# Kernel optimization log

Hardware: AMD Instinct MI355X
Metric: run time of the kernel (lower is better)

The kernel has to match this reference:

```python
import jax, jax.numpy as jnp
import numpy as np


def _shift(w):
    # max(0, -min(w)): scalar shift making w + shift non-negative
    return jnp.maximum(0.0, -jnp.min(w))


def shifted_linear(x, W, b=None):
    # F.linear with non-negative weights plus row-sum correction
    alpha = _shift(W)
    y = x @ (W + alpha).T - alpha * jnp.sum(x, axis=-1, keepdims=True)
    if b is not None:
        y = y + b
    return y


def shifted_depthwise_conv(x, w, b):
    # x: (B, D, L), w: (D, 1, K) depthwise; causal-style padding K-1, sliced to L by caller
    alpha = _shift(w)
    k = w.shape[2]
    pad = k - 1
    dn = ('NCH', 'OIH', 'NCH')
    groups = w.shape[0]
    y = jax.lax.conv_general_dilated(x, w + alpha, (1,), [(pad, pad)],
                                     dimension_numbers=dn, feature_group_count=groups)
    ones_k = jnp.ones_like(w)
    ssum = jax.lax.conv_general_dilated(x, ones_k, (1,), [(pad, pad)],
                                        dimension_numbers=dn, feature_group_count=groups)
    return y - alpha * ssum + b[None, :, None]


def setup_inputs() -> dict:
    key = jax.random.key(0)
    ks = jax.random.split(key, 10)
    d_model, d_inner, d_state, d_conv, dt_rank = 1024, 2048, 16, 4, 64
    B, L = 2, 1024
    s = 0.05
    return {
        'hidden_states': jax.random.normal(ks[0], (B, L, d_model), jnp.float32),
        'W_in': jax.random.normal(ks[1], (2 * d_inner, d_model), jnp.float32) * s,
        'conv_w': jax.random.normal(ks[2], (d_inner, 1, d_conv), jnp.float32) * 0.3,
        'conv_b': jax.random.normal(ks[3], (d_inner,), jnp.float32) * s,
        'W_x': jax.random.normal(ks[4], (dt_rank + 2 * d_state, d_inner), jnp.float32) * s,
        'W_dt': jax.random.normal(ks[5], (d_inner, dt_rank), jnp.float32) * s,
        'dt_bias': jax.random.normal(ks[6], (d_inner,), jnp.float32),
        'W_out': jax.random.normal(ks[7], (d_model, d_inner), jnp.float32) * s,
        'A_log': jax.random.normal(ks[8], (d_inner, d_state), jnp.float32) * 0.5,
        'D': jax.random.normal(ks[9], (d_inner,), jnp.float32),
    }


def reference(hidden_states, W_in, conv_w, conv_b, W_x, W_dt, dt_bias, W_out, A_log, D):
    b, l, dm = hidden_states.shape
    d_inner = conv_w.shape[0]
    d_state = A_log.shape[1]
    dt_rank = W_dt.shape[1]

    A = jnp.exp(A_log)  # (d_inner, d_state), always positive

    # in_proj over (b*l, d_model) -> (b, 2*d_inner, l)
    xz = shifted_linear(hidden_states.reshape(b * l, dm), W_in)
    xz = xz.reshape(b, l, 2 * d_inner).transpose(0, 2, 1)
    x, z = xz[:, :d_inner], xz[:, d_inner:]

    # depthwise shifted conv + SiLU activation, truncated to seqlen
    x = jax.nn.silu(shifted_depthwise_conv(x, conv_w, conv_b)[..., :l])

    # x_proj -> dt_raw, B, C
    x_dbl = shifted_linear(x.transpose(0, 2, 1).reshape(b * l, d_inner), W_x)
    dt_raw = x_dbl[:, :dt_rank]
    Bm = x_dbl[:, dt_rank:dt_rank + d_state].reshape(b, l, d_state).transpose(0, 2, 1)  # (b,n,l)
    Cm = x_dbl[:, dt_rank + d_state:].reshape(b, l, d_state).transpose(0, 2, 1)         # (b,n,l)
    dt = shifted_linear(dt_raw, W_dt).reshape(b, l, d_inner).transpose(0, 2, 1)          # (b,d,l)

    # delta activation (softplus) with bias, clamped
    delta = jnp.clip(jax.nn.softplus(dt + dt_bias[None, :, None]), 1e-4, 20.0)

    # global scalar shifts for B and C
    beta = _shift(Bm)
    gamma = _shift(Cm)
    B_nn = Bm + beta
    C_nn = Cm + gamma

    # precomputed per-step operands, scan axis first: (l, b, d, n)
    deltaA = jnp.exp(-jnp.einsum('bdl,dn->lbdn', delta, A))
    dBu = jnp.einsum('bdl,bnl,bdl->lbdn', delta, B_nn, x)
    C_scan = C_nn.transpose(2, 0, 1)  # (l, b, n)

    def step(xc, inp):
        dA_i, dBu_i, C_i = inp
        xc = dA_i * xc + dBu_i                                   # (b,d,n)
        y = jnp.einsum('bdn,bn->bd', xc, C_i) - gamma * jnp.sum(xc, axis=-1)
        return xc, y

    x0 = jnp.zeros((b, d_inner, d_state), dtype=delta.dtype)
    _, ys = jax.lax.scan(step, x0, (deltaA, dBu, C_scan))        # ys: (l, b, d)

    y = ys.transpose(1, 2, 0) + x * D[None, :, None]             # (b, d, l) skip term
    y = y * jax.nn.silu(z)                                       # gate activation

    out = shifted_linear(y.transpose(0, 2, 1).reshape(b * l, d_inner), W_out)
    return out.reshape(b, l, dm)
```

## Files before the change

### kernel.cpp

```cpp
#include <hip/hip_runtime.h>
#include <hip/hip_bf16.h>
#include <math.h>

#define DM 1024
#define DI 2048
#define DS 16
#define DTR 64
#define NB 2
#define LL 1024
#define TT (NB*LL)
#define SCH 32
#define NCH (LL/SCH)

typedef unsigned short u16;
typedef __attribute__((ext_vector_type(8))) short bf16x8;
typedef __attribute__((ext_vector_type(4))) float f32x4;

#define LOG2E 1.4426950408889634f

__device__ inline u16 f2bf(float f) {
  union { float f; unsigned u; } c; c.f = f;
  unsigned u = c.u;
  return (u16)((u + 0x7fffu + ((u >> 16) & 1u)) >> 16);
}
__device__ inline float bf2f(u16 u) {
  union { unsigned u; float f; } c; c.u = ((unsigned)u) << 16;
  return c.f;
}

__device__ inline unsigned fkey(float f) {
  union { float f; unsigned u; } c; c.f = f;
  return (c.u & 0x80000000u) ? ~c.u : (c.u | 0x80000000u);
}
__device__ inline float funkey(unsigned k) {
  union { unsigned u; float f; } c;
  c.u = (k & 0x80000000u) ? (k & 0x7fffffffu) : ~k;
  return c.f;
}

#define GLDS16(g, l) __builtin_amdgcn_global_load_lds( \
    (const __attribute__((address_space(1))) unsigned int*)(g), \
    (__attribute__((address_space(3))) unsigned int*)(l), 16, 0, 0)

template<int BM, int BN, int EPI, int OB, int CG = 0>
__global__ __launch_bounds__(256) void gemm_bf16(
    const u16* __restrict__ A, const u16* __restrict__ B,
    void* __restrict__ Cv, int M, int N, int K, int kpb,
    const float* __restrict__ bias) {
  constexpr int WAVES_M = BM / 64;
  constexpr int WAVES_N = 4 / WAVES_M;
  constexpr int WTM = 4;
  constexpr int WTN = BN / (WAVES_N * 16);
  constexpr int ASLABS = BM / 16;
  constexpr int SLABS = (BM + BN) / 16;
  constexpr int SPW = SLABS / 4;
  __shared__ u16 As[BM * 32];
  __shared__ u16 Bs[BN * 32];
  const int tid = threadIdx.x;
  const int wave = tid >> 6;
  const int lane = tid & 63;
  const int bm = blockIdx.y * BM;
  const int bn = blockIdx.x * BN;
  const int wm = (wave / WAVES_N) * 64;
  const int wn = (wave % WAVES_N) * (WTN * 16);
  const int r4 = lane >> 2;
  const int kc = (lane & 3) * 8;
  const int fr = lane & 15;
  const int fq = lane >> 4;
  const int koff = blockIdx.z * kpb;
  float* C = (float*)Cv + (OB == 0 ? (size_t)blockIdx.z * M * N : (size_t)0);
  u16* C16 = (u16*)Cv;

  f32x4 acc[WTM][WTN];
#pragma unroll
  for (int i = 0; i < WTM; ++i)
#pragma unroll
    for (int j = 0; j < WTN; ++j) acc[i][j] = (f32x4){0.f, 0.f, 0.f, 0.f};

  for (int k0 = koff; k0 < koff + kpb; k0 += 32) {
#pragma unroll
    for (int s = wave * SPW; s < (wave + 1) * SPW; ++s) {
      if (s < ASLABS) {
        int row = s * 16 + r4;
        GLDS16(A + (size_t)(bm + row) * K + k0 + kc, &As[s * 512]);
      } else {
        int row = (s - ASLABS) * 16 + r4;
        GLDS16(B + (size_t)(bn + row) * K + k0 + kc, &Bs[(s - ASLABS) * 512]);
      }
    }
    __syncthreads();
    bf16x8 af[WTM], bf[WTN];
#pragma unroll
    for (int i = 0; i < WTM; ++i)
      af[i] = *(const bf16x8*)&As[(wm + 16 * i + fr) * 32 + fq * 8];
#pragma unroll
    for (int j = 0; j < WTN; ++j)
      bf[j] = *(const bf16x8*)&Bs[(wn + 16 * j + fr) * 32 + fq * 8];
#pragma unroll
    for (int i = 0; i < WTM; ++i)
#pragma unroll
      for (int j = 0; j < WTN; ++j)
        acc[i][j] = __builtin_amdgcn_mfma_f32_16x16x32_bf16(af[i], bf[j], acc[i][j], 0, 0, 0);
    __syncthreads();
  }

#pragma unroll
  for (int i = 0; i < WTM; ++i) {
    int row0 = bm + wm + 16 * i + fq * 4;
#pragma unroll
    for (int j = 0; j < WTN; ++j) {
      int col = bn + wn + 16 * j + fr;
#pragma unroll
      for (int r = 0; r < 4; ++r) {
        float v = acc[i][j][r];
        if (EPI == 1) {
          v += bias[col];
          float sp = (v > 20.0f) ? v : log1pf(expf(v));
          v = fminf(fmaxf(sp, 1e-4f), 20.0f);
        }
        if (OB == 1) {
          C16[(size_t)(row0 + r) * N + col] = f2bf(v);
        } else if (OB == 2) {
          if (CG == 0 || col < CG) {
            const int ldc = (CG > 0) ? CG : N;
            atomicAdd(&C[(size_t)(row0 + r) * ldc + col], v);
          }
        } else {
          C[(size_t)(row0 + r) * N + col] = v;
        }
      }
    }
  }
}

__global__ __launch_bounds__(256) void dtbeta(
    const float* __restrict__ xdb, u16* __restrict__ dtraw_bf,
    unsigned* __restrict__ betakey) {
  const int t0 = blockIdx.x * 32;
  const int tid = threadIdx.x;
#pragma unroll
  for (int i = tid; i < 32 * 64; i += 256) {
    int t = t0 + (i >> 6), c = i & 63;
    dtraw_bf[t * 64 + c] = f2bf(xdb[t * 96 + c]);
  }
  float mn = 3.4e38f;
#pragma unroll
  for (int i = tid; i < 32 * 16; i += 256) {
    int t = t0 + (i >> 4), n = i & 15;
    mn = fminf(mn, xdb[t * 96 + 64 + n]);
  }
#pragma unroll
  for (int o = 32; o; o >>= 1) mn = fminf(mn, __shfl_down(mn, o));
  __shared__ float sm[4];
  if ((tid & 63) == 0) sm[tid >> 6] = mn;
  __syncthreads();
  if (tid == 0) {
    float m = fminf(fminf(sm[0], sm[1]), fminf(sm[2], sm[3]));
    atomicMin(betakey, fkey(m));
  }
}

__global__ __launch_bounds__(256) void cast_all(
    const float* __restrict__ hs, const float* __restrict__ win,
    const float* __restrict__ wout, const float* __restrict__ wx,
    const float* __restrict__ wdt,
    u16* __restrict__ hs_bf, u16* __restrict__ win_bf,
    u16* __restrict__ wout_bf, u16* __restrict__ wx_bf,
    u16* __restrict__ wdt_bf, float* __restrict__ xdb,
    float* __restrict__ outz, unsigned* __restrict__ betakey) {
  int gid = blockIdx.x * 256 + threadIdx.x;
  if (gid == 0) betakey[0] = 0xFFFFFFFFu;
  const float* src; u16* dst; int off;
  if (gid < 524288)       { src = hs;   dst = hs_bf;   off = gid; }
  else if (gid < 1572864) { src = win;  dst = win_bf;  off = gid - 524288; }
  else if (gid < 2097152) { src = wout; dst = wout_bf; off = gid - 1572864; }
  else if (gid < 2146304) { src = wx;   dst = wx_bf;   off = gid - 2097152; }
  else if (gid < 2179072) { src = wdt;  dst = wdt_bf;  off = gid - 2146304; }
  else if (gid < 2195456) {
    ushort4 z4 = {0, 0, 0, 0};
    ((ushort4*)wx_bf)[49152 + gid - 2179072] = z4;
    return;
  } else if (gid < 2244608) {
    float4 z = {0.f, 0.f, 0.f, 0.f};
    ((float4*)xdb)[gid - 2195456] = z;
    return;
  } else {
    float4 z = {0.f, 0.f, 0.f, 0.f};
    ((float4*)outz)[gid - 2244608] = z;
    return;
  }
  float4 v = ((const float4*)src)[off];
  ushort4 o;
  o.x = f2bf(v.x); o.y = f2bf(v.y); o.z = f2bf(v.z); o.w = f2bf(v.w);
  ((ushort4*)dst)[off] = o;
}

__global__ __launch_bounds__(256) void conv_silu4(
    const u16* __restrict__ xz, const float* __restrict__ w,
    const float* __restrict__ cb, u16* __restrict__ xc_bf) {
  int gid = blockIdx.x * 256 + threadIdx.x;
  int dq = (gid & 511) * 4;
  int t = gid >> 9;
  int l = t & (LL - 1);
  float wv[4][4];
#pragma unroll
  for (int j = 0; j < 4; ++j) {
    float4 ww = *(const float4*)&w[(dq + j) * 4];
    wv[j][0] = ww.x; wv[j][1] = ww.y; wv[j][2] = ww.z; wv[j][3] = ww.w;
  }
  float4 acc = *(const float4*)&cb[dq];
#pragma unroll
  for (int k = 0; k < 4; ++k) {
    int ll = l - 3 + k;
    if (ll < 0) continue;
    ushort4 xv = *(const ushort4*)&xz[(size_t)(t - 3 + k) * (2 * DI) + dq];
    acc.x += bf2f(xv.x) * wv[0][k]; acc.y += bf2f(xv.y) * wv[1][k];
    acc.z += bf2f(xv.z) * wv[2][k]; acc.w += bf2f(xv.w) * wv[3][k];
  }
  acc.x /= (1.0f + expf(-acc.x)); acc.y /= (1.0f + expf(-acc.y));
  acc.z /= (1.0f + expf(-acc.z)); acc.w /= (1.0f + expf(-acc.w));
  ushort4 o;
  o.x = f2bf(acc.x); o.y = f2bf(acc.y); o.z = f2bf(acc.z); o.w = f2bf(acc.w);
  *(ushort4*)&xc_bf[(size_t)t * DI + dq] = o;
}

__global__ __launch_bounds__(256) void scan_pass1(
    const u16* __restrict__ delta, const u16* __restrict__ xc_bf,
    const float* __restrict__ xdb, const float* __restrict__ A_log,
    const unsigned* __restrict__ betak,
    float* __restrict__ hend, float* __restrict__ Ssum) {
  const int d = blockIdx.x * 256 + threadIdx.x;
  const int c = blockIdx.y;
  const int b = blockIdx.z;
  __shared__ float Bsh[SCH][16];
  const float beta = fmaxf(0.0f, -funkey(betak[0]));
  const int t0 = b * LL + c * SCH;
  for (int i = threadIdx.x; i < SCH * 16; i += 256) {
    int tt = i >> 4, n = i & 15;
    Bsh[tt][n] = xdb[(size_t)(t0 + tt) * 96 + 64 + n] + beta;
  }
  __syncthreads();
  float Av2[16];
#pragma unroll
  for (int n = 0; n < 16; ++n) Av2[n] = expf(A_log[d * 16 + n]) * LOG2E;
  float h[16];
#pragma unroll
  for (int n = 0; n < 16; ++n) h[n] = 0.f;
  float S = 0.f;
  for (int tt = 0; tt < SCH; ++tt) {
    int t = t0 + tt;
    float dv = bf2f(delta[(size_t)t * DI + d]);
    float xv = bf2f(xc_bf[(size_t)t * DI + d]);
    float dx = dv * xv;
    S += dv;
#pragma unroll
    for (int n = 0; n < 16; ++n) {
      float a = __builtin_amdgcn_exp2f(-dv * Av2[n]);
      h[n] = a * h[n] + dx * Bsh[tt][n];
    }
  }
  size_t base = (((size_t)(b * NCH + c) * DI) + d) * 16;
#pragma unroll
  for (int n = 0; n < 16; ++n) hend[base + n] = h[n];
  Ssum[((size_t)(b * NCH + c) * DI) + d] = S;
}

__global__ __launch_bounds__(256) void scan_pass2(
    float* __restrict__ hend, const float* __restrict__ Ssum,
    const float* __restrict__ A_log) {
  int gid = blockIdx.x * 256 + threadIdx.x;
  int n = gid & 15;
  int d = (gid >> 4) & (DI - 1);
  int b = gid >> 15;
  float Av2 = expf(A_log[d * 16 + n]) * LOG2E;
  float H = 0.f;
  for (int c = 0; c < NCH; ++c) {
    size_t cb = ((size_t)(b * NCH + c) * DI) + d;
    float hl = hend[cb * 16 + n];
    float p = __builtin_amdgcn_exp2f(-Av2 * Ssum[cb]);
    hend[cb * 16 + n] = H;
    H = p * H + hl;
  }
}

__global__ __launch_bounds__(256) void scan_pass3(
    const u16* __restrict__ delta, const u16* __restrict__ xc_bf,
    const float* __restrict__ xdb, const u16* __restrict__ xz_bf,
    const float* __restrict__ A_log, const float* __restrict__ Dp,
    const unsigned* __restrict__ betak, const float* __restrict__ hstart,
    u16* __restrict__ ybf) {
  const int d = blockIdx.x * 256 + threadIdx.x;
  const int c = blockIdx.y;
  const int b = blockIdx.z;
  __shared__ float Bsh[SCH][16];
  __shared__ float Csh[SCH][16];
  const float beta = fmaxf(0.0f, -funkey(betak[0]));
  const int t0 = b * LL + c * SCH;
  for (int i = threadIdx.x; i < SCH * 16; i += 256) {
    int tt = i >> 4, n = i & 15;
    size_t row = (size_t)(t0 + tt) * 96;
    Bsh[tt][n] = xdb[row + 64 + n] + beta;
    Csh[tt][n] = xdb[row + 80 + n];
  }
  __syncthreads();
  float Av2[16];
#pragma unroll
  for (int n = 0; n < 16; ++n) Av2[n] = expf(A_log[d * 16 + n]) * LOG2E;
  float h[16];
  size_t base = (((size_t)(b * NCH + c) * DI) + d) * 16;
#pragma unroll
  for (int n = 0; n < 16; ++n) h[n] = hstart[base + n];
  const float Dd = Dp[d];
  for (int tt = 0; tt < SCH; ++tt) {
    int t = t0 + tt;
    float dv = bf2f(delta[(size_t)t * DI + d]);
    float xv = bf2f(xc_bf[(size_t)t * DI + d]);
    float dx = dv * xv;
    float yv = 0.f;
#pragma unroll
    for (int n = 0; n < 16; ++n) {
      float a = __builtin_amdgcn_exp2f(-dv * Av2[n]);
      h[n] = a * h[n] + dx * Bsh[tt][n];
      yv += h[n] * Csh[tt][n];
    }
    float zv = bf2f(xz_bf[(size_t)t * (2 * DI) + DI + d]);
    float out = (yv + xv * Dd) * (zv / (1.0f + expf(-zv)));
    ybf[(size_t)t * DI + d] = f2bf(out);
  }
}

extern "C" void kernel_launch(void* const* d_in, const int* in_sizes, int n_in,
                              void* d_out, int out_size, void* d_ws, size_t ws_size,
                              hipStream_t stream) {
  const float* hs      = (const float*)d_in[0];
  const float* W_in    = (const float*)d_in[1];
  const float* conv_w  = (const float*)d_in[2];
  const float* conv_b  = (const float*)d_in[3];
  const float* W_x     = (const float*)d_in[4];
  const float* W_dt    = (const float*)d_in[5];
  const float* dt_bias = (const float*)d_in[6];
  const float* W_out   = (const float*)d_in[7];
  const float* A_log   = (const float*)d_in[8];
  const float* Dp      = (const float*)d_in[9];
  float* out = (float*)d_out;

  float* ws       = (float*)d_ws;
  float* xz_bfR   = ws;
  float* xcv_bfR  = xz_bfR + (size_t)TT * 2 * DI / 2;
  float* xdb      = xcv_bfR + (size_t)TT * DI / 2;
  float* dlt_bfR  = xdb + (size_t)TT * 96;
  float* betab    = dlt_bfR + (size_t)TT * DI / 2;
  float* hend     = betab + 64;
  float* Ssum     = hend + (size_t)NB * NCH * DI * 16;
  float* hs_bfR   = Ssum + (size_t)NB * NCH * DI;
  float* win_bfR  = hs_bfR + (size_t)TT * DM / 2;
  float* wout_bfR = win_bfR + (size_t)2 * DI * DM / 2;
  float* wx_bfR   = wout_bfR + (size_t)DM * DI / 2;
  float* wdt_bfR  = wx_bfR + 131072;
  float* dtraw_bfR = wdt_bfR + 65536;

  u16* xz_bf    = (u16*)xz_bfR;
  u16* xcv_bf   = (u16*)xcv_bfR;
  u16* dlt_bf   = (u16*)dlt_bfR;
  u16* hs_bf    = (u16*)hs_bfR;
  u16* win_bf   = (u16*)win_bfR;
  u16* wout_bf  = (u16*)wout_bfR;
  u16* wx_bf    = (u16*)wx_bfR;
  u16* wdt_bf   = (u16*)wdt_bfR;
  u16* dtraw_bf = (u16*)dtraw_bfR;
  unsigned* betakey = (unsigned*)betab;
  u16* ybf      = (u16*)win_bfR;

  dim3 blk(256);

  cast_all<<<10816, blk, 0, stream>>>(hs, W_in, W_out, W_x, W_dt,
                                      hs_bf, win_bf, wout_bf, wx_bf, wdt_bf,
                                      xdb, out, betakey);

  gemm_bf16<128, 128, 0, 1><<<dim3(4096 / 128, TT / 128), blk, 0, stream>>>(
      hs_bf, win_bf, xz_bf, TT, 2 * DI, DM, DM, nullptr);

  conv_silu4<<<(TT * DI / 4) / 256, blk, 0, stream>>>(xz_bf, conv_w, conv_b, xcv_bf);

  gemm_bf16<64, 128, 0, 2, 96><<<dim3(1, TT / 64, 8), blk, 0, stream>>>(
      xcv_bf, wx_bf, xdb, TT, 128, DI, DI / 8, nullptr);

  dtbeta<<<64, blk, 0, stream>>>(xdb, dtraw_bf, betakey);

  gemm_bf16<64, 128, 1, 1><<<dim3(DI / 128, TT / 64), blk, 0, stream>>>(
      dtraw_bf, wdt_bf, dlt_bf, TT, DI, DTR, DTR, dt_bias);

  scan_pass1<<<dim3(DI / 256, NCH, NB), blk, 0, stream>>>(
      dlt_bf, xcv_bf, xdb, A_log, betakey, hend, Ssum);
  scan_pass2<<<(NB * DI * DS) / 256, blk, 0, stream>>>(hend, Ssum, A_log);
  scan_pass3<<<dim3(DI / 256, NCH, NB), blk, 0, stream>>>(
      dlt_bf, xcv_bf, xdb, xz_bf, A_log, Dp, betakey, hend, ybf);

  gemm_bf16<128, 128, 0, 2, 0><<<dim3(DM / 128, TT / 128, 4), blk, 0, stream>>>(
      ybf, wout_bf, out, TT, DM, DI, DI / 4, nullptr);
}
```

Baseline: 264.0 us.

## Fuse weight casts into GEMM loads, drop scan pass2 and dtbeta kernels

W_x, W_dt and W_out are now converted from fp32 to bf16 inside the GEMM tile loads instead of in a separate cast pass. The dt projection reads raw xdb with lda 96, and its first 64 blocks also compute the beta minimum, which removes the dtbeta kernel. Scan pass2 is folded into pass3: each chunk serially recombines the states of all earlier chunks, costing O(c) redundant work per chunk. The x_proj split-K is widened to 16 slices. The goal is fewer launches and less fp32 cast traffic, at the cost of register-staged loads replacing direct-to-LDS loads and extra exp2 work in the scan.

Result: slower. 313.2 us (+18.6%).

```diff
diff --git a/kernel.cpp b/kernel.cpp
--- a/kernel.cpp
+++ b/kernel.cpp
@@ -1,5 +1,4 @@
 #include <hip/hip_runtime.h>
-#include <hip/hip_bf16.h>
 #include <math.h>
 
 #define DM 1024
@@ -38,15 +37,26 @@
   return c.f;
 }
 
+__device__ inline bf16x8 cvt8(float4 a, float4 b) {
+  bf16x8 w;
+  w[0] = (short)f2bf(a.x); w[1] = (short)f2bf(a.y);
+  w[2] = (short)f2bf(a.z); w[3] = (short)f2bf(a.w);
+  w[4] = (short)f2bf(b.x); w[5] = (short)f2bf(b.y);
+  w[6] = (short)f2bf(b.z); w[7] = (short)f2bf(b.w);
+  return w;
+}
+
 #define GLDS16(g, l) __builtin_amdgcn_global_load_lds( \
     (const __attribute__((address_space(1))) unsigned int*)(g), \
     (__attribute__((address_space(3))) unsigned int*)(l), 16, 0, 0)
 
-template<int BM, int BN, int EPI, int OB, int CG = 0>
-__global__ __launch_bounds__(256) void gemm_bf16(
-    const u16* __restrict__ A, const u16* __restrict__ B,
-    void* __restrict__ Cv, int M, int N, int K, int kpb,
-    const float* __restrict__ bias) {
+template<int BM, int BN, int EPI, int OB, int CGd, int ASRC, int BSRC,
+         int BVAL, int BMIN>
+__global__ __launch_bounds__(256) void gemm_k(
+    const void* __restrict__ Av, const void* __restrict__ Bv,
+    void* __restrict__ Cv, int M, int N, int K, int lda, int ldb, int kpb,
+    const float* __restrict__ bias,
+    const float* __restrict__ minsrc, unsigned* __restrict__ betakey) {
   constexpr int WAVES_M = BM / 64;
   constexpr int WAVES_N = 4 / WAVES_M;
   constexpr int WTM = 4;
@@ -56,6 +66,7 @@
   constexpr int SPW = SLABS / 4;
   __shared__ u16 As[BM * 32];
   __shared__ u16 Bs[BN * 32];
+  __shared__ float sm4[4];
   const int tid = threadIdx.x;
   const int wave = tid >> 6;
   const int lane = tid & 63;
@@ -68,8 +79,27 @@
   const int fr = lane & 15;
   const int fq = lane >> 4;
   const int koff = blockIdx.z * kpb;
-  float* C = (float*)Cv + (OB == 0 ? (size_t)blockIdx.z * M * N : (size_t)0);
+  float* C = (float*)Cv;
   u16* C16 = (u16*)Cv;
+
+  if constexpr (BMIN == 1) {
+    int fb = blockIdx.y * gridDim.x + blockIdx.x;
+    if (fb < 64) {
+      const int t0 = fb * 32;
+      float mn = 3.4e38f;
+      for (int i = tid; i < 32 * 16; i += 256) {
+        int t = t0 + (i >> 4), n = i & 15;
+        mn = fminf(mn, minsrc[t * 96 + 64 + n]);
+      }
+#pragma unroll
+      for (int o = 32; o; o >>= 1) mn = fminf(mn, __shfl_down(mn, o));
+      if ((tid & 63) == 0) sm4[tid >> 6] = mn;
+      __syncthreads();
+      if (tid == 0)
+        atomicMin(betakey, fkey(fminf(fminf(sm4[0], sm4[1]), fminf(sm4[2], sm4[3]))));
+      __syncthreads();
+    }
+  }
 
   f32x4 acc[WTM][WTN];
 #pragma unroll
@@ -82,10 +112,31 @@
     for (int s = wave * SPW; s < (wave + 1) * SPW; ++s) {
       if (s < ASLABS) {
         int row = s * 16 + r4;
-        GLDS16(A + (size_t)(bm + row) * K + k0 + kc, &As[s * 512]);
+        if constexpr (ASRC == 0) {
+          GLDS16((const u16*)Av + (size_t)(bm + row) * lda + k0 + kc, &As[s * 512]);
+        } else {
+          const float* src = (const float*)Av + (size_t)(bm + row) * lda + k0 + kc;
+          float4 v0 = *(const float4*)src;
+          float4 v1 = *(const float4*)(src + 4);
+          *(bf16x8*)&As[s * 512 + lane * 8] = cvt8(v0, v1);
+        }
       } else {
-        int row = (s - ASLABS) * 16 + r4;
-        GLDS16(B + (size_t)(bn + row) * K + k0 + kc, &Bs[(s - ASLABS) * 512]);
+        int bs = s - ASLABS;
+        int row = bs * 16 + r4;
+        if constexpr (BSRC == 0) {
+          GLDS16((const u16*)Bv + (size_t)(bn + row) * ldb + k0 + kc, &Bs[bs * 512]);
+        } else {
+          bf16x8 w;
+#pragma unroll
+          for (int q = 0; q < 8; ++q) w[q] = 0;
+          if (BVAL == 0 || (bn + row) < BVAL) {
+            const float* src = (const float*)Bv + (size_t)(bn + row) * ldb + k0 + kc;
+            float4 v0 = *(const float4*)src;
+            float4 v1 = *(const float4*)(src + 4);
+            w = cvt8(v0, v1);
+          }
+          *(bf16x8*)&Bs[bs * 512 + lane * 8] = w;
+        }
       }
     }
     __syncthreads();
@@ -120,73 +171,34 @@
         }
         if (OB == 1) {
           C16[(size_t)(row0 + r) * N + col] = f2bf(v);
-        } else if (OB == 2) {
-          if (CG == 0 || col < CG) {
-            const int ldc = (CG > 0) ? CG : N;
+        } else {
+          if (CGd == 0 || col < CGd) {
+            const int ldc = (CGd > 0) ? CGd : N;
             atomicAdd(&C[(size_t)(row0 + r) * ldc + col], v);
           }
-        } else {
-          C[(size_t)(row0 + r) * N + col] = v;
         }
       }
     }
   }
 }
 
-__global__ __launch_bounds__(256) void dtbeta(
-    const float* __restrict__ xdb, u16* __restrict__ dtraw_bf,
+__global__ __launch_bounds__(256) void cast2(
+    const float* __restrict__ hs, const float* __restrict__ win,
+    u16* __restrict__ hs_bf, u16* __restrict__ win_bf,
+    float* __restrict__ xdb, float* __restrict__ outz,
     unsigned* __restrict__ betakey) {
-  const int t0 = blockIdx.x * 32;
-  const int tid = threadIdx.x;
-#pragma unroll
-  for (int i = tid; i < 32 * 64; i += 256) {
-    int t = t0 + (i >> 6), c = i & 63;
-    dtraw_bf[t * 64 + c] = f2bf(xdb[t * 96 + c]);
-  }
-  float mn = 3.4e38f;
-#pragma unroll
-  for (int i = tid; i < 32 * 16; i += 256) {
-    int t = t0 + (i >> 4), n = i & 15;
-    mn = fminf(mn, xdb[t * 96 + 64 + n]);
-  }
-#pragma unroll
-  for (int o = 32; o; o >>= 1) mn = fminf(mn, __shfl_down(mn, o));
-  __shared__ float sm[4];
-  if ((tid & 63) == 0) sm[tid >> 6] = mn;
-  __syncthreads();
-  if (tid == 0) {
-    float m = fminf(fminf(sm[0], sm[1]), fminf(sm[2], sm[3]));
-    atomicMin(betakey, fkey(m));
-  }
-}
-
-__global__ __launch_bounds__(256) void cast_all(
-    const float* __restrict__ hs, const float* __restrict__ win,
-    const float* __restrict__ wout, const float* __restrict__ wx,
-    const float* __restrict__ wdt,
-    u16* __restrict__ hs_bf, u16* __restrict__ win_bf,
-    u16* __restrict__ wout_bf, u16* __restrict__ wx_bf,
-    u16* __restrict__ wdt_bf, float* __restrict__ xdb,
-    float* __restrict__ outz, unsigned* __restrict__ betakey) {
   int gid = blockIdx.x * 256 + threadIdx.x;
   if (gid == 0) betakey[0] = 0xFFFFFFFFu;
   const float* src; u16* dst; int off;
-  if (gid < 524288)       { src = hs;   dst = hs_bf;   off = gid; }
-  else if (gid < 1572864) { src = win;  dst = win_bf;  off = gid - 524288; }
-  else if (gid < 2097152) { src = wout; dst = wout_bf; off = gid - 1572864; }
-  else if (gid < 2146304) { src = wx;   dst = wx_bf;   off = gid - 2097152; }
-  else if (gid < 2179072) { src = wdt;  dst = wdt_bf;  off = gid - 2146304; }
-  else if (gid < 2195456) {
-    ushort4 z4 = {0, 0, 0, 0};
-    ((ushort4*)wx_bf)[49152 + gid - 2179072] = z4;
-    return;
-  } else if (gid < 2244608) {
+  if (gid < 524288)       { src = hs;  dst = hs_bf;  off = gid; }
+  else if (gid < 1572864) { src = win; dst = win_bf; off = gid - 524288; }
+  else if (gid < 1622016) {
     float4 z = {0.f, 0.f, 0.f, 0.f};
-    ((float4*)xdb)[gid - 2195456] = z;
+    ((float4*)xdb)[gid - 1572864] = z;
     return;
   } else {
     float4 z = {0.f, 0.f, 0.f, 0.f};
-    ((float4*)outz)[gid - 2244608] = z;
+    ((float4*)outz)[gid - 1622016] = z;
     return;
   }
   float4 v = ((const float4*)src)[off];
@@ -265,30 +277,12 @@
   Ssum[((size_t)(b * NCH + c) * DI) + d] = S;
 }
 
-__global__ __launch_bounds__(256) void scan_pass2(
-    float* __restrict__ hend, const float* __restrict__ Ssum,
-    const float* __restrict__ A_log) {
-  int gid = blockIdx.x * 256 + threadIdx.x;
-  int n = gid & 15;
-  int d = (gid >> 4) & (DI - 1);
-  int b = gid >> 15;
-  float Av2 = expf(A_log[d * 16 + n]) * LOG2E;
-  float H = 0.f;
-  for (int c = 0; c < NCH; ++c) {
-    size_t cb = ((size_t)(b * NCH + c) * DI) + d;
-    float hl = hend[cb * 16 + n];
-    float p = __builtin_amdgcn_exp2f(-Av2 * Ssum[cb]);
-    hend[cb * 16 + n] = H;
-    H = p * H + hl;
-  }
-}
-
-__global__ __launch_bounds__(256) void scan_pass3(
+__global__ __launch_bounds__(256) void scan_pass3p(
     const u16* __restrict__ delta, const u16* __restrict__ xc_bf,
     const float* __restrict__ xdb, const u16* __restrict__ xz_bf,
     const float* __restrict__ A_log, const float* __restrict__ Dp,
-    const unsigned* __restrict__ betak, const float* __restrict__ hstart,
-    u16* __restrict__ ybf) {
+    const unsigned* __restrict__ betak, const float* __restrict__ hloc,
+    const float* __restrict__ Ssum, u16* __restrict__ ybf) {
   const int d = blockIdx.x * 256 + threadIdx.x;
   const int c = blockIdx.y;
   const int b = blockIdx.z;
@@ -307,9 +301,23 @@
 #pragma unroll
   for (int n = 0; n < 16; ++n) Av2[n] = expf(A_log[d * 16 + n]) * LOG2E;
   float h[16];
-  size_t base = (((size_t)(b * NCH + c) * DI) + d) * 16;
-#pragma unroll
-  for (int n = 0; n < 16; ++n) h[n] = hstart[base + n];
+#pragma unroll
+  for (int n = 0; n < 16; ++n) h[n] = 0.f;
+  for (int j = 0; j < c; ++j) {
+    size_t cb = ((size_t)(b * NCH + j) * DI) + d;
+    float S = Ssum[cb];
+    const float4* hl = (const float4*)&hloc[cb * 16];
+    float hv[16];
+    *(float4*)&hv[0]  = hl[0];
+    *(float4*)&hv[4]  = hl[1];
+    *(float4*)&hv[8]  = hl[2];
+    *(float4*)&hv[12] = hl[3];
+#pragma unroll
+    for (int n = 0; n < 16; ++n) {
+      float pr = __builtin_amdgcn_exp2f(-Av2[n] * S);
+      h[n] = pr * h[n] + hv[n];
+    }
+  }
   const float Dd = Dp[d];
   for (int tt = 0; tt < SCH; ++tt) {
     int t = t0 + tt;
@@ -324,8 +332,8 @@
       yv += h[n] * Csh[tt][n];
     }
     float zv = bf2f(xz_bf[(size_t)t * (2 * DI) + DI + d]);
-    float out = (yv + xv * Dd) * (zv / (1.0f + expf(-zv)));
-    ybf[(size_t)t * DI + d] = f2bf(out);
+    float outv = (yv + xv * Dd) * (zv / (1.0f + expf(-zv)));
+    ybf[(size_t)t * DI + d] = f2bf(outv);
   }
 }
 
@@ -354,48 +362,40 @@
   float* Ssum     = hend + (size_t)NB * NCH * DI * 16;
   float* hs_bfR   = Ssum + (size_t)NB * NCH * DI;
   float* win_bfR  = hs_bfR + (size_t)TT * DM / 2;
-  float* wout_bfR = win_bfR + (size_t)2 * DI * DM / 2;
-  float* wx_bfR   = wout_bfR + (size_t)DM * DI / 2;
-  float* wdt_bfR  = wx_bfR + 131072;
-  float* dtraw_bfR = wdt_bfR + 65536;
-
-  u16* xz_bf    = (u16*)xz_bfR;
-  u16* xcv_bf   = (u16*)xcv_bfR;
-  u16* dlt_bf   = (u16*)dlt_bfR;
-  u16* hs_bf    = (u16*)hs_bfR;
-  u16* win_bf   = (u16*)win_bfR;
-  u16* wout_bf  = (u16*)wout_bfR;
-  u16* wx_bf    = (u16*)wx_bfR;
-  u16* wdt_bf   = (u16*)wdt_bfR;
-  u16* dtraw_bf = (u16*)dtraw_bfR;
+
+  u16* xz_bf   = (u16*)xz_bfR;
+  u16* xcv_bf  = (u16*)xcv_bfR;
+  u16* dlt_bf  = (u16*)dlt_bfR;
+  u16* hs_bf   = (u16*)hs_bfR;
+  u16* win_bf  = (u16*)win_bfR;
   unsigned* betakey = (unsigned*)betab;
-  u16* ybf      = (u16*)win_bfR;
+  u16* ybf     = (u16*)win_bfR;
 
   dim3 blk(256);
 
-  cast_all<<<10816, blk, 0, stream>>>(hs, W_in, W_out, W_x, W_dt,
-                                      hs_bf, win_bf, wout_bf, wx_bf, wdt_bf,
-                                      xdb, out, betakey);
-
-  gemm_bf16<128, 128, 0, 1><<<dim3(4096 / 128, TT / 128), blk, 0, stream>>>(
-      hs_bf, win_bf, xz_bf, TT, 2 * DI, DM, DM, nullptr);
+  cast2<<<8384, blk, 0, stream>>>(hs, W_in, hs_bf, win_bf, xdb, out, betakey);
+
+  gemm_k<128, 128, 0, 1, 0, 0, 0, 0, 0>
+      <<<dim3(4096 / 128, TT / 128), blk, 0, stream>>>(
+      hs_bf, win_bf, xz_bf, TT, 2 * DI, DM, DM, DM, DM, nullptr, nullptr, nullptr);
 
   conv_silu4<<<(TT * DI / 4) / 256, blk, 0, stream>>>(xz_bf, conv_w, conv_b, xcv_bf);
 
-  gemm_bf16<64, 128, 0, 2, 96><<<dim3(1, TT / 64, 8), blk, 0, stream>>>(
-      xcv_bf, wx_bf, xdb, TT, 128, DI, DI / 8, nullptr);
-
-  dtbeta<<<64, blk, 0, stream>>>(xdb, dtraw_bf, betakey);
-
-  gemm_bf16<64, 128, 1, 1><<<dim3(DI / 128, TT / 64), blk, 0, stream>>>(
-      dtraw_bf, wdt_bf, dlt_bf, TT, DI, DTR, DTR, dt_bias);
+  gemm_k<64, 128, 0, 2, 96, 0, 1, 96, 0>
+      <<<dim3(1, TT / 64, 16), blk, 0, stream>>>(
+      xcv_bf, W_x, xdb, TT, 128, DI, DI, DI, DI / 16, nullptr, nullptr, nullptr);
+
+  gemm_k<64, 128, 1, 1, 0, 1, 1, 0, 1>
+      <<<dim3(DI / 128, TT / 64), blk, 0, stream>>>(
+      xdb, W_dt, dlt_bf, TT, DI, DTR, 96, DTR, DTR, dt_bias, xdb, betakey);
 
   scan_pass1<<<dim3(DI / 256, NCH, NB), blk, 0, stream>>>(
       dlt_bf, xcv_bf, xdb, A_log, betakey, hend, Ssum);
-  scan_pass2<<<(NB * DI * DS) / 256, blk, 0, stream>>>(hend, Ssum, A_log);
-  scan_pass3<<<dim3(DI / 256, NCH, NB), blk, 0, stream>>>(
-      dlt_bf, xcv_bf, xdb, xz_bf, A_log, Dp, betakey, hend, ybf);
-
-  gemm_bf16<128, 128, 0, 2, 0><<<dim3(DM / 128, TT / 128, 4), blk, 0, stream>>>(
-      ybf, wout_bf, out, TT, DM, DI, DI / 4, nullptr);
-}
+
+  scan_pass3p<<<dim3(DI / 256, NCH, NB), blk, 0, stream>>>(
+      dlt_bf, xcv_bf, xdb, xz_bf, A_log, Dp, betakey, hend, Ssum, ybf);
+
+  gemm_k<128, 128, 0, 2, 0, 0, 1, 0, 0>
+      <<<dim3(DM / 128, TT / 128, 4), blk, 0, stream>>>(
+      ybf, W_out, out, TT, DM, DI, DI, DI, DI / 4, nullptr, nullptr, nullptr);
+}
```
